# Performance work log

Hardware: AMD Instinct MI355X
Metric: run time of the kernel (lower is better)

The kernel has to match this reference:

```python
import jax, jax.numpy as jnp
import numpy as np

N = 100000      # nodes
E = 1600000     # directed edges (bidirectional pairs)
DIN = 64
DOUT = 64
T = 3
LMBDA = 0.5
EPS = 1e-9


def setup_inputs() -> dict:
    key = jax.random.key(0)
    k1, k2, k3, k4 = jax.random.split(key, 4)
    x = jax.random.normal(k1, (N, DIN), dtype=jnp.float32)
    Eh = E // 2
    s = jax.random.randint(k2, (Eh,), 0, N)
    d = jax.random.randint(k3, (Eh,), 0, N)
    # bidirectional layout required by assert_bidirectional:
    # row0 = [s, d], row1 = [d, s]
    edge_index = jnp.stack([jnp.concatenate([s, d]), jnp.concatenate([d, s])]).astype(jnp.int32)
    W = jax.random.normal(k4, (DIN, DOUT), dtype=jnp.float32) / np.sqrt(DIN)
    b = jnp.zeros((DOUT,), dtype=jnp.float32)
    lmbda = jnp.float32(LMBDA)
    return {"x": x, "edge_index": edge_index, "W": W, "b": b, "lmbda": lmbda}


def _ema(h, src, dst, lmbda):
    # h: [N, D] node features after linear; src/dst: [E] int
    Eh = src.shape[0] // 2
    deg = jax.ops.segment_sum(jnp.ones(src.shape[0], h.dtype), src, num_segments=N)  # [N]
    h_e = h[src]                       # [E, D]  (expand)
    deg_e = deg[src][:, None]          # [E, 1]
    M = h_e                            # initial edge messages M_ij = x_i
    m = jax.ops.segment_sum(M, dst, num_segments=N)  # [N, D]  (aggregate)
    coef = lmbda / (deg_e - 1.0 + EPS)

    def step(carry, _):
        M, m = carry
        m_e = m[src]                                   # [E, D]
        M_ji = jnp.roll(M, -Eh, axis=0)                # reversed-edge messages
        M_new = jnp.where(deg_e == 1.0, h_e,
                          (1.0 - lmbda) * h_e + coef * (m_e - M_ji))
        m_new = jax.ops.segment_sum(M_new, dst, num_segments=N)
        return (M_new, m_new), None

    (M, m), _ = jax.lax.scan(step, (M, m), None, length=T)
    degN = deg[:, None]
    return jnp.where(degN == 0.0, h,
                     (1.0 - lmbda) * h + lmbda / (degN + EPS) * m)


def reference(x, edge_index, W, b, lmbda):
    src, dst = edge_index[0], edge_index[1]
    x_in = x                       # dim_in == dim_out -> residual uses pre-linear x
    h = x @ W + b                  # pyg_nn.Linear
    y = jax.nn.relu(_ema(h, src, dst, lmbda))
    # dropout p=0.0 (eval) is identity
    return x_in + y
```

## Files before the change

kernel.cpp:

```cpp
#include <hip/hip_runtime.h>
#include <hip/hip_bf16.h>


static __device__ __forceinline__ float bf2f(unsigned short v) {
    union { unsigned int u; float f; } x;
    x.u = ((unsigned int)v) << 16;
    return x.f;
}

static __device__ __forceinline__ unsigned short f2bf(float f) {
    union { unsigned int u; float f; } x;
    x.f = f;
    unsigned int r = x.u + 0x7FFFu + ((x.u >> 16) & 1u);
    return (unsigned short)(r >> 16);
}

static __device__ __forceinline__ float edge_c(int dm1) {
    float fd = (float)dm1;
    float raw = 0.5f * __builtin_amdgcn_rcpf(fd);
    return (fd == 0.0f) ? 0.0f : raw;
}

__global__ void ema_gemm_kernel(const float* __restrict__ x, const float* __restrict__ W,
                                const float* __restrict__ bias, unsigned short* __restrict__ hbf) {
    int wave = (int)((blockIdx.x * 256 + threadIdx.x) >> 6);
    int lane = (int)(threadIdx.x & 63);
    int n0 = wave * 8;
    if (n0 >= 100000) return;
    float w[64];
    #pragma unroll
    for (int k = 0; k < 64; ++k) w[k] = W[k * 64 + lane];
    float bv = bias[lane];
    int nend = (n0 + 8 < 100000) ? (n0 + 8) : 100000;
    for (int n = n0; n < nend; ++n) {
        const float* xr = x + (size_t)__builtin_amdgcn_readfirstlane(n) * 64;
        float acc = bv;
        #pragma unroll
        for (int k = 0; k < 64; ++k) acc = fmaf(xr[k], w[k], acc);
        hbf[n * 64 + lane] = f2bf(acc);
    }
}

__global__ void ema_hist_kernel(const int* ei, int* hcnt) {
    __shared__ int hist[391];
    int t = (int)threadIdx.x;
    int bl = (int)blockIdx.x;
    for (int i = t; i < 391; i += 256) hist[i] = 0;
    __syncthreads();
    int e0 = bl * 4096;
    #pragma unroll
    for (int i = 0; i < 16; ++i) {
        int e = e0 + t + i * 256;
        if (e < 1600000) {
            int dst = (e < 800000) ? ei[e + 800000] : ei[e - 800000];
            atomicAdd(&hist[dst >> 8], 1);
        }
    }
    __syncthreads();
    for (int i = t; i < 391; i += 256) hcnt[i * 391 + bl] = hist[i];
}

__global__ void ema_bscan_row_kernel(int* hcnt, int* btot) {
    __shared__ int s[512];
    int bu = (int)blockIdx.x;
    int t = (int)threadIdx.x;
    int v = (t < 391) ? hcnt[bu * 391 + t] : 0;
    s[t] = v;
    __syncthreads();
    for (int off = 1; off < 512; off <<= 1) {
        int add = (t >= off) ? s[t - off] : 0;
        __syncthreads();
        s[t] += add;
        __syncthreads();
    }
    if (t < 391) hcnt[bu * 391 + t] = s[t] - v;
    if (t == 390) btot[bu] = s[t];
}

__global__ void ema_bscan_base_kernel(const int* btot, int* bbase) {
    __shared__ int s[512];
    int t = (int)threadIdx.x;
    int v = (t < 391) ? btot[t] : 0;
    s[t] = v;
    __syncthreads();
    for (int off = 1; off < 512; off <<= 1) {
        int add = (t >= off) ? s[t - off] : 0;
        __syncthreads();
        s[t] += add;
        __syncthreads();
    }
    if (t < 391) bbase[t] = s[t] - v;
    if (t == 390) bbase[391] = s[t];
}

__global__ void ema_scatter_kernel(const int* ei, const int* hcnt,
                                   const int* bbase, unsigned int* stage) {
    __shared__ int base[391];
    __shared__ int cnt[391];
    int t = (int)threadIdx.x;
    int bl = (int)blockIdx.x;
    for (int i = t; i < 391; i += 256) {
        base[i] = hcnt[i * 391 + bl] + bbase[i];
        cnt[i] = 0;
    }
    __syncthreads();
    int e0 = bl * 4096;
    #pragma unroll
    for (int i = 0; i < 16; ++i) {
        int e = e0 + t + i * 256;
        if (e < 1600000) {
            int src = ei[e];
            int dst = (e < 800000) ? ei[e + 800000] : ei[e - 800000];
            int bu = dst >> 8;
            int slot = base[bu] + atomicAdd(&cnt[bu], 1);
            stage[slot] = ((unsigned int)(dst & 255) << 24) | (unsigned int)src;
        }
    }
}

__global__ void ema_fillcsr_count_kernel(const int* __restrict__ bbase,
                                         const unsigned int* __restrict__ stage,
                                         int* __restrict__ degi,
                                         int* __restrict__ rs) {
    __shared__ int cnt[256];
    __shared__ int scn[256];
    int b = (int)blockIdx.x;
    int t = (int)threadIdx.x;
    cnt[t] = 0;
    __syncthreads();
    int seg_lo = bbase[b];
    int seg_hi = bbase[b + 1];
    for (int i = seg_lo + t; i < seg_hi; i += 256) {
        atomicAdd(&cnt[stage[i] >> 24], 1);
    }
    __syncthreads();
    int v = cnt[t];
    scn[t] = v;
    __syncthreads();
    for (int off = 1; off < 256; off <<= 1) {
        int add = (t >= off) ? scn[t - off] : 0;
        __syncthreads();
        scn[t] += add;
        __syncthreads();
    }
    int node = (b << 8) + t;
    if (node < 100000) {
        degi[node] = v;
        rs[node] = seg_lo + scn[t] - v;
    }
}

__global__ void ema_fillcsr_write_kernel(const int* __restrict__ rs,
                                         const unsigned int* __restrict__ stage,
                                         const int* __restrict__ degi,
                                         int* __restrict__ csr,
                                         float* __restrict__ cf) {
    __shared__ int rsl[256];
    __shared__ int cnt[256];
    int b = (int)blockIdx.x;
    int t = (int)threadIdx.x;
    int node_lo = b << 8;
    int node = node_lo + t;
    rsl[t] = (node < 100000) ? rs[node] : 1600000;
    cnt[t] = 0;
    __syncthreads();
    int seg_lo = rsl[0];
    int seg_hi = (node_lo + 256 < 100000) ? rs[node_lo + 256] : 1600000;
    for (int i = seg_lo + t; i < seg_hi; i += 256) {
        unsigned int v = stage[i];
        int local = (int)(v >> 24);
        int srcn = (int)(v & 0x00FFFFFFu);
        int dm1 = degi[srcn] - 1;
        if (dm1 < 0) dm1 = 0;
        if (dm1 > 32767) dm1 = 32767;
        int slot = rsl[local] + atomicAdd(&cnt[local], 1);
        csr[slot] = (dm1 << 17) | srcn;
        cf[slot] = edge_c(dm1);
    }
}

__global__ void ema_cfcopy_kernel(const float4* __restrict__ cf4,
                                  float4* __restrict__ cfD4) {
    int i = (int)(blockIdx.x * 256 + threadIdx.x);
    if (i < 400000) cfD4[i] = cf4[i];
}

__global__ void ema_passA_kernel(const int* __restrict__ degi, const int* __restrict__ rs,
                                 const int* __restrict__ csr, const float* __restrict__ cf,
                                 const unsigned short* __restrict__ hbf,
                                 unsigned short* __restrict__ m0, unsigned short* __restrict__ W1,
                                 unsigned short* __restrict__ W2, unsigned short* __restrict__ W3a,
                                 float2* __restrict__ pp) {
    int wid = (int)((blockIdx.x * 256 + threadIdx.x) >> 6);
    int c = (int)(threadIdx.x & 63);
    if (wid >= 100000) return;
    int dv = __builtin_amdgcn_readfirstlane(degi[wid]);
    int base = wid * 64 + c;
    float hv = bf2f(hbf[base]);
    if (dv == 0) {
        m0[base] = 0;
        W1[base] = 0;
        W2[base] = 0;
        W3a[base] = f2bf(hv);
        if (c == 0) pp[wid] = make_float2(0.0f, 0.0f);
        return;
    }
    int j = __builtin_amdgcn_readfirstlane(rs[wid]);
    int end = j + dv;
    float av = (dv > 1) ? 0.5f : 1.0f;
    float cv = (dv > 1) ? 0.5f / ((float)dv - 1.0f + 1e-9f) : 0.0f;
    float fv = av * hv;
    float sm = 0.0f, sS = 0.0f, sQ = 0.0f, p1 = 0.0f, p2 = 0.0f;
    for (; j + 4 <= end; j += 4) {
        unsigned int w0 = (unsigned int)csr[j];
        unsigned int w1 = (unsigned int)csr[j + 1];
        unsigned int w2 = (unsigned int)csr[j + 2];
        unsigned int w3 = (unsigned int)csr[j + 3];
        int a0 = (int)(w0 & 0x1FFFFu), d0 = (int)(w0 >> 17);
        int a1 = (int)(w1 & 0x1FFFFu), d1 = (int)(w1 >> 17);
        int a2 = (int)(w2 & 0x1FFFFu), d2 = (int)(w2 >> 17);
        int a3 = (int)(w3 & 0x1FFFFu), d3 = (int)(w3 >> 17);
        float c0 = cf[j], c1 = cf[j + 1], c2 = cf[j + 2], c3 = cf[j + 3];
        float h0 = bf2f(hbf[a0 * 64 + c]);
        float h1 = bf2f(hbf[a1 * 64 + c]);
        float h2 = bf2f(hbf[a2 * 64 + c]);
        float h3 = bf2f(hbf[a3 * 64 + c]);
        float al0 = d0 ? 0.5f : 1.0f;
        float al1 = d1 ? 0.5f : 1.0f;
        float al2 = d2 ? 0.5f : 1.0f;
        float al3 = d3 ? 0.5f : 1.0f;
        sm += (h0 + h1) + (h2 + h3);
        sS += al0 * h0 + al1 * h1 + al2 * h2 + al3 * h3;
        sQ += c0 * h0 + c1 * h1 + c2 * h2 + c3 * h3;
        p1 += (c0 + c1) + (c2 + c3);
        p2 += c0 * c0 + c1 * c1 + c2 * c2 + c3 * c3;
    }
    for (; j < end; ++j) {
        unsigned int w0 = (unsigned int)csr[j];
        int a = (int)(w0 & 0x1FFFFu), d0 = (int)(w0 >> 17);
        float ha = bf2f(hbf[a * 64 + c]);
        float ca = cf[j];
        float ala = d0 ? 0.5f : 1.0f;
        sm += ha;
        sS += ala * ha;
        sQ += ca * ha;
        p1 += ca;
        p2 += ca * ca;
    }
    float r = 0.5f / ((float)dv + 1e-9f);
    float w1o = sS - hv * p1;
    float w2o = sS - fv * p1 - cv * p1 * sm + cv * sQ;
    float w3o = 0.5f * hv + r * (sS - fv * p1 + 0.5f * cv * sQ - cv * hv * p2);
    m0[base] = f2bf(sm);
    W1[base] = f2bf(w1o);
    W2[base] = f2bf(w2o);
    W3a[base] = f2bf(w3o);
    if (c == 0) pp[wid] = make_float2(r * cv * p1, r * cv);
}

__global__ void ema_passB_kernel(const int* __restrict__ degi, const int* __restrict__ rs,
                                 const int* __restrict__ csr, const float* __restrict__ cf,
                                 const unsigned short* __restrict__ m0,
                                 unsigned short* __restrict__ W1m1, unsigned short* __restrict__ W3W4,
                                 const float2* __restrict__ pp) {
    int wid = (int)((blockIdx.x * 256 + threadIdx.x) >> 6);
    int c = (int)(threadIdx.x & 63);
    if (wid >= 100000) return;
    int dv = __builtin_amdgcn_readfirstlane(degi[wid]);
    if (dv == 0) return;
    int base = wid * 64 + c;
    int j = __builtin_amdgcn_readfirstlane(rs[wid]);
    int end = j + dv;
    float t1 = 0.0f, t2 = 0.0f;
    for (; j + 4 <= end; j += 4) {
        unsigned int w0 = (unsigned int)csr[j];
        unsigned int w1 = (unsigned int)csr[j + 1];
        unsigned int w2 = (unsigned int)csr[j + 2];
        unsigned int w3 = (unsigned int)csr[j + 3];
        int a0 = (int)(w0 & 0x1FFFFu);
        int a1 = (int)(w1 & 0x1FFFFu);
        int a2 = (int)(w2 & 0x1FFFFu);
        int a3 = (int)(w3 & 0x1FFFFu);
        float c0 = cf[j], c1 = cf[j + 1], c2 = cf[j + 2], c3 = cf[j + 3];
        float m0v = bf2f(m0[a0 * 64 + c]);
        float m1v = bf2f(m0[a1 * 64 + c]);
        float m2v = bf2f(m0[a2 * 64 + c]);
        float m3v = bf2f(m0[a3 * 64 + c]);
        t1 += c0 * m0v + c1 * m1v + c2 * m2v + c3 * m3v;
        t2 += c0 * c0 * m0v + c1 * c1 * m1v + c2 * c2 * m2v + c3 * c3 * m3v;
    }
    for (; j < end; ++j) {
        unsigned int w0 = (unsigned int)csr[j];
        int a = (int)(w0 & 0x1FFFFu);
        float ca = cf[j];
        float mv = bf2f(m0[a * 64 + c]);
        t1 += ca * mv;
        t2 += ca * ca * mv;
    }
    float2 ppv = pp[wid];
    float m1 = bf2f(W1m1[base]) + t1;
    float w4 = bf2f(W3W4[base]) - ppv.x * m1 + ppv.y * t2;
    W1m1[base] = f2bf(m1);
    W3W4[base] = f2bf(w4);
}

__global__ void ema_passC_kernel(const int* __restrict__ degi, const int* __restrict__ rs,
                                 const int* __restrict__ csr, const float* __restrict__ cf,
                                 const unsigned short* __restrict__ m1,
                                 unsigned short* __restrict__ W2m2) {
    int wid = (int)((blockIdx.x * 256 + threadIdx.x) >> 6);
    int c = (int)(threadIdx.x & 63);
    if (wid >= 100000) return;
    int dv = __builtin_amdgcn_readfirstlane(degi[wid]);
    if (dv == 0) return;
    int base = wid * 64 + c;
    int j = __builtin_amdgcn_readfirstlane(rs[wid]);
    int end = j + dv;
    float t = 0.0f;
    for (; j + 4 <= end; j += 4) {
        unsigned int w0 = (unsigned int)csr[j];
        unsigned int w1 = (unsigned int)csr[j + 1];
        unsigned int w2 = (unsigned int)csr[j + 2];
        unsigned int w3 = (unsigned int)csr[j + 3];
        int a0 = (int)(w0 & 0x1FFFFu);
        int a1 = (int)(w1 & 0x1FFFFu);
        int a2 = (int)(w2 & 0x1FFFFu);
        int a3 = (int)(w3 & 0x1FFFFu);
        float c0 = cf[j], c1 = cf[j + 1], c2 = cf[j + 2], c3 = cf[j + 3];
        float m0v = bf2f(m1[a0 * 64 + c]);
        float m1v = bf2f(m1[a1 * 64 + c]);
        float m2v = bf2f(m1[a2 * 64 + c]);
        float m3v = bf2f(m1[a3 * 64 + c]);
        t += c0 * m0v + c1 * m1v + c2 * m2v + c3 * m3v;
    }
    for (; j < end; ++j) {
        unsigned int w0 = (unsigned int)csr[j];
        int a = (int)(w0 & 0x1FFFFu);
        t += cf[j] * bf2f(m1[a * 64 + c]);
    }
    float m2v = bf2f(W2m2[base]) + t;
    W2m2[base] = f2bf(m2v);
}

__global__ void GraphEMALayer_18133351924067_kernel(
    const int* __restrict__ degi, const int* __restrict__ rs,
    const int* __restrict__ csr, const float* __restrict__ cfD,
    const unsigned short* __restrict__ m2, const unsigned short* __restrict__ W4,
    const float* __restrict__ x, float* __restrict__ out) {
    int wid = (int)((blockIdx.x * 256 + threadIdx.x) >> 6);
    int c = (int)(threadIdx.x & 63);
    if (wid >= 100000) return;
    int dv = __builtin_amdgcn_readfirstlane(degi[wid]);
    int base = wid * 64 + c;
    float xv = x[base];
    float y = bf2f(W4[base]);
    if (dv > 0) {
        int j = __builtin_amdgcn_readfirstlane(rs[wid]);
        int end = j + dv;
        float t = 0.0f;
        for (; j + 4 <= end; j += 4) {
            unsigned int w0 = (unsigned int)csr[j];
            unsigned int w1 = (unsigned int)csr[j + 1];
            unsigned int w2 = (unsigned int)csr[j + 2];
            unsigned int w3 = (unsigned int)csr[j + 3];
            int a0 = (int)(w0 & 0x1FFFFu);
            int a1 = (int)(w1 & 0x1FFFFu);
            int a2 = (int)(w2 & 0x1FFFFu);
            int a3 = (int)(w3 & 0x1FFFFu);
            float c0 = cfD[j], c1 = cfD[j + 1], c2 = cfD[j + 2], c3 = cfD[j + 3];
            float m0v = bf2f(m2[a0 * 64 + c]);
            float m1v = bf2f(m2[a1 * 64 + c]);
            float m2v = bf2f(m2[a2 * 64 + c]);
            float m3v = bf2f(m2[a3 * 64 + c]);
            t += c0 * m0v + c1 * m1v + c2 * m2v + c3 * m3v;
        }
        for (; j < end; ++j) {
            unsigned int w0 = (unsigned int)csr[j];
            int a = (int)(w0 & 0x1FFFFu);
            t += cfD[j] * bf2f(m2[a * 64 + c]);
        }
        float r = 0.5f / ((float)dv + 1e-9f);
        y += r * t;
    }
    if (y < 0.0f) y = 0.0f;
    out[base] = xv + y;
}

extern "C" void kernel_launch(void* const* d_in, const int* in_sizes, int n_in,
                              void* d_out, int out_size, void* d_ws, size_t ws_size,
                              hipStream_t stream) {
    (void)in_sizes; (void)n_in; (void)out_size; (void)ws_size;

    const float* x    = (const float*)d_in[0];
    const int*   ei   = (const int*)d_in[1];
    const float* W    = (const float*)d_in[2];
    const float* bias = (const float*)d_in[3];
    float* out = (float*)d_out;
    unsigned short* m0 = (unsigned short*)d_out;
    float* cf = (float*)((char*)d_out + 12800000);

    char* ws = (char*)d_ws;
    unsigned short* hbf  = (unsigned short*)(ws);
    unsigned short* W1m1 = (unsigned short*)(ws + 12800000);
    unsigned short* W2m2 = (unsigned short*)(ws + 25600000);
    unsigned short* W3W4 = (unsigned short*)(ws + 38400000);
    int* degi = (int*)(ws + 51200000);
    int* rs   = (int*)(ws + 51600000);
    float2* pp   = (float2*)(ws + 52800000);
    int* csr  = (int*)(ws + 53600000);
    int* bbase = (int*)(ws + 60000000);
    int* btot  = (int*)(ws + 60002048);

    unsigned int* stage = (unsigned int*)(ws + 12800000);
    int* hcnt = (int*)(ws + 25600000);
    float* cfD = (float*)(ws);

    int eb = (100000 * 64 + 255) / 256;
    int nb = (100000 + 255) / 256;
    int pb = (1600000 + 4095) / 4096;
    int gb = (100000 + 31) / 32;
    int cb = (400000 + 255) / 256;

    ema_gemm_kernel<<<gb, 256, 0, stream>>>(x, W, bias, hbf);

    ema_hist_kernel<<<pb, 256, 0, stream>>>(ei, hcnt);
    ema_bscan_row_kernel<<<391, 512, 0, stream>>>(hcnt, btot);
    ema_bscan_base_kernel<<<1, 512, 0, stream>>>(btot, bbase);
    ema_scatter_kernel<<<pb, 256, 0, stream>>>(ei, hcnt, bbase, stage);
    ema_fillcsr_count_kernel<<<nb, 256, 0, stream>>>(bbase, stage, degi, rs);
    ema_fillcsr_write_kernel<<<nb, 256, 0, stream>>>(rs, stage, degi, csr, cf);

    ema_passA_kernel<<<eb, 256, 0, stream>>>(degi, rs, csr, cf, hbf,
                                             m0, W1m1, W2m2, W3W4, pp);
    ema_cfcopy_kernel<<<cb, 256, 0, stream>>>((const float4*)cf, (float4*)cfD);
    ema_passB_kernel<<<eb, 256, 0, stream>>>(degi, rs, csr, cf, m0,
                                             W1m1, W3W4, pp);
    ema_passC_kernel<<<eb, 256, 0, stream>>>(degi, rs, csr, cf, W1m1, W2m2);
    GraphEMALayer_18133351924067_kernel<<<eb, 256, 0, stream>>>(
        degi, rs, csr, cfD, W2m2, W3W4, x, out);
}
```

Baseline: 387.3 us.

## Merge CSR count/write, precompute edge coefficients and squared coefficients, unroll gathers by eight

The two CSR fill kernels are merged into one that keeps the row starts in shared memory, and the packed degree bits are dropped from csr. A new kernel computes per-edge coefficients and their squares, and another computes the per-node p1/p2 sums with wave reductions, which moves that work out of passA. The gather loops in all passes are unrolled to 8 edges to keep more loads in flight. This adds two kernel launches and an extra cf2 array read in passB, in exchange for fewer serial dependencies and less per-edge arithmetic.

```diff
diff --git a/kernel.cpp b/kernel.cpp
--- a/kernel.cpp
+++ b/kernel.cpp
@@ -118,12 +118,14 @@
     }
 }
 
-__global__ void ema_fillcsr_count_kernel(const int* __restrict__ bbase,
-                                         const unsigned int* __restrict__ stage,
-                                         int* __restrict__ degi,
-                                         int* __restrict__ rs) {
+__global__ void ema_fillcsr_kernel(const int* __restrict__ bbase,
+                                   const unsigned int* __restrict__ stage,
+                                   int* __restrict__ degi,
+                                   int* __restrict__ rs,
+                                   int* __restrict__ csr) {
     __shared__ int cnt[256];
     __shared__ int scn[256];
+    __shared__ int rsl[256];
     int b = (int)blockIdx.x;
     int t = (int)threadIdx.x;
     cnt[t] = 0;
@@ -143,40 +145,58 @@
         scn[t] += add;
         __syncthreads();
     }
+    int start = seg_lo + scn[t] - v;
+    rsl[t] = start;
     int node = (b << 8) + t;
     if (node < 100000) {
         degi[node] = v;
-        rs[node] = seg_lo + scn[t] - v;
-    }
-}
-
-__global__ void ema_fillcsr_write_kernel(const int* __restrict__ rs,
-                                         const unsigned int* __restrict__ stage,
-                                         const int* __restrict__ degi,
-                                         int* __restrict__ csr,
-                                         float* __restrict__ cf) {
-    __shared__ int rsl[256];
-    __shared__ int cnt[256];
-    int b = (int)blockIdx.x;
-    int t = (int)threadIdx.x;
-    int node_lo = b << 8;
-    int node = node_lo + t;
-    rsl[t] = (node < 100000) ? rs[node] : 1600000;
+        rs[node] = start;
+    }
     cnt[t] = 0;
     __syncthreads();
-    int seg_lo = rsl[0];
-    int seg_hi = (node_lo + 256 < 100000) ? rs[node_lo + 256] : 1600000;
     for (int i = seg_lo + t; i < seg_hi; i += 256) {
-        unsigned int v = stage[i];
-        int local = (int)(v >> 24);
-        int srcn = (int)(v & 0x00FFFFFFu);
-        int dm1 = degi[srcn] - 1;
-        if (dm1 < 0) dm1 = 0;
-        if (dm1 > 32767) dm1 = 32767;
+        unsigned int s = stage[i];
+        int local = (int)(s >> 24);
+        int srcn = (int)(s & 0x00FFFFFFu);
         int slot = rsl[local] + atomicAdd(&cnt[local], 1);
-        csr[slot] = (dm1 << 17) | srcn;
-        cf[slot] = edge_c(dm1);
-    }
+        csr[slot] = srcn;
+    }
+}
+
+__global__ void ema_cfgen_kernel(const int* __restrict__ csr,
+                                 const int* __restrict__ degi,
+                                 float* __restrict__ cf,
+                                 float* __restrict__ cf2) {
+    int i = (int)(blockIdx.x * 256 + threadIdx.x);
+    if (i >= 1600000) return;
+    int dm1 = degi[csr[i]] - 1;
+    float v = edge_c(dm1);
+    cf[i] = v;
+    cf2[i] = v * v;
+}
+
+__global__ void ema_p12_kernel(const int* __restrict__ degi, const int* __restrict__ rs,
+                               const float* __restrict__ cf, float2* __restrict__ P12) {
+    int wid = (int)((blockIdx.x * 256 + threadIdx.x) >> 6);
+    int lane = (int)(threadIdx.x & 63);
+    if (wid >= 100000) return;
+    int dv = __builtin_amdgcn_readfirstlane(degi[wid]);
+    if (dv == 0) {
+        if (lane == 0) P12[wid] = make_float2(0.0f, 0.0f);
+        return;
+    }
+    int j0 = __builtin_amdgcn_readfirstlane(rs[wid]);
+    float p1 = 0.0f, p2 = 0.0f;
+    for (int l = lane; l < dv; l += 64) {
+        float cv = cf[j0 + l];
+        p1 += cv;
+        p2 += cv * cv;
+    }
+    for (int off = 32; off > 0; off >>= 1) {
+        p1 += __shfl_xor(p1, off);
+        p2 += __shfl_xor(p2, off);
+    }
+    if (lane == 0) P12[wid] = make_float2(p1, p2);
 }
 
 __global__ void ema_cfcopy_kernel(const float4* __restrict__ cf4,
@@ -187,6 +207,7 @@
 
 __global__ void ema_passA_kernel(const int* __restrict__ degi, const int* __restrict__ rs,
                                  const int* __restrict__ csr, const float* __restrict__ cf,
+                                 const float2* __restrict__ P12,
                                  const unsigned short* __restrict__ hbf,
                                  unsigned short* __restrict__ m0, unsigned short* __restrict__ W1,
                                  unsigned short* __restrict__ W2, unsigned short* __restrict__ W3a,
@@ -210,42 +231,59 @@
     float av = (dv > 1) ? 0.5f : 1.0f;
     float cv = (dv > 1) ? 0.5f / ((float)dv - 1.0f + 1e-9f) : 0.0f;
     float fv = av * hv;
-    float sm = 0.0f, sS = 0.0f, sQ = 0.0f, p1 = 0.0f, p2 = 0.0f;
+    float2 p12 = P12[wid];
+    float p1 = p12.x, p2 = p12.y;
+    float sm = 0.0f, sS = 0.0f, sQ = 0.0f;
+    for (; j + 8 <= end; j += 8) {
+        int a0 = csr[j],     a1 = csr[j + 1], a2 = csr[j + 2], a3 = csr[j + 3];
+        int a4 = csr[j + 4], a5 = csr[j + 5], a6 = csr[j + 6], a7 = csr[j + 7];
+        float c0 = cf[j],     c1 = cf[j + 1], c2 = cf[j + 2], c3 = cf[j + 3];
+        float c4 = cf[j + 4], c5 = cf[j + 5], c6 = cf[j + 6], c7 = cf[j + 7];
+        float h0 = bf2f(hbf[a0 * 64 + c]);
+        float h1 = bf2f(hbf[a1 * 64 + c]);
+        float h2 = bf2f(hbf[a2 * 64 + c]);
+        float h3 = bf2f(hbf[a3 * 64 + c]);
+        float h4 = bf2f(hbf[a4 * 64 + c]);
+        float h5 = bf2f(hbf[a5 * 64 + c]);
+        float h6 = bf2f(hbf[a6 * 64 + c]);
+        float h7 = bf2f(hbf[a7 * 64 + c]);
+        float al0 = (c0 == 0.0f) ? 1.0f : 0.5f;
+        float al1 = (c1 == 0.0f) ? 1.0f : 0.5f;
+        float al2 = (c2 == 0.0f) ? 1.0f : 0.5f;
+        float al3 = (c3 == 0.0f) ? 1.0f : 0.5f;
+        float al4 = (c4 == 0.0f) ? 1.0f : 0.5f;
+        float al5 = (c5 == 0.0f) ? 1.0f : 0.5f;
+        float al6 = (c6 == 0.0f) ? 1.0f : 0.5f;
+        float al7 = (c7 == 0.0f) ? 1.0f : 0.5f;
+        sm += ((h0 + h1) + (h2 + h3)) + ((h4 + h5) + (h6 + h7));
+        sS += (al0 * h0 + al1 * h1 + al2 * h2 + al3 * h3)
+            + (al4 * h4 + al5 * h5 + al6 * h6 + al7 * h7);
+        sQ += (c0 * h0 + c1 * h1 + c2 * h2 + c3 * h3)
+            + (c4 * h4 + c5 * h5 + c6 * h6 + c7 * h7);
+    }
     for (; j + 4 <= end; j += 4) {
-        unsigned int w0 = (unsigned int)csr[j];
-        unsigned int w1 = (unsigned int)csr[j + 1];
-        unsigned int w2 = (unsigned int)csr[j + 2];
-        unsigned int w3 = (unsigned int)csr[j + 3];
-        int a0 = (int)(w0 & 0x1FFFFu), d0 = (int)(w0 >> 17);
-        int a1 = (int)(w1 & 0x1FFFFu), d1 = (int)(w1 >> 17);
-        int a2 = (int)(w2 & 0x1FFFFu), d2 = (int)(w2 >> 17);
-        int a3 = (int)(w3 & 0x1FFFFu), d3 = (int)(w3 >> 17);
+        int a0 = csr[j], a1 = csr[j + 1], a2 = csr[j + 2], a3 = csr[j + 3];
         float c0 = cf[j], c1 = cf[j + 1], c2 = cf[j + 2], c3 = cf[j + 3];
         float h0 = bf2f(hbf[a0 * 64 + c]);
         float h1 = bf2f(hbf[a1 * 64 + c]);
         float h2 = bf2f(hbf[a2 * 64 + c]);
         float h3 = bf2f(hbf[a3 * 64 + c]);
-        float al0 = d0 ? 0.5f : 1.0f;
-        float al1 = d1 ? 0.5f : 1.0f;
-        float al2 = d2 ? 0.5f : 1.0f;
-        float al3 = d3 ? 0.5f : 1.0f;
+        float al0 = (c0 == 0.0f) ? 1.0f : 0.5f;
+        float al1 = (c1 == 0.0f) ? 1.0f : 0.5f;
+        float al2 = (c2 == 0.0f) ? 1.0f : 0.5f;
+        float al3 = (c3 == 0.0f) ? 1.0f : 0.5f;
         sm += (h0 + h1) + (h2 + h3);
         sS += al0 * h0 + al1 * h1 + al2 * h2 + al3 * h3;
         sQ += c0 * h0 + c1 * h1 + c2 * h2 + c3 * h3;
-        p1 += (c0 + c1) + (c2 + c3);
-        p2 += c0 * c0 + c1 * c1 + c2 * c2 + c3 * c3;
     }
     for (; j < end; ++j) {
-        unsigned int w0 = (unsigned int)csr[j];
-        int a = (int)(w0 & 0x1FFFFu), d0 = (int)(w0 >> 17);
+        int a = csr[j];
+        float ca = cf[j];
         float ha = bf2f(hbf[a * 64 + c]);
-        float ca = cf[j];
-        float ala = d0 ? 0.5f : 1.0f;
+        float ala = (ca == 0.0f) ? 1.0f : 0.5f;
         sm += ha;
         sS += ala * ha;
         sQ += ca * ha;
-        p1 += ca;
-        p2 += ca * ca;
     }
     float r = 0.5f / ((float)dv + 1e-9f);
     float w1o = sS - hv * p1;
@@ -260,6 +298,7 @@
 
 __global__ void ema_passB_kernel(const int* __restrict__ degi, const int* __restrict__ rs,
                                  const int* __restrict__ csr, const float* __restrict__ cf,
+                                 const float* __restrict__ cf2,
                                  const unsigned short* __restrict__ m0,
                                  unsigned short* __restrict__ W1m1, unsigned short* __restrict__ W3W4,
                                  const float2* __restrict__ pp) {
@@ -272,30 +311,42 @@
     int j = __builtin_amdgcn_readfirstlane(rs[wid]);
     int end = j + dv;
     float t1 = 0.0f, t2 = 0.0f;
+    for (; j + 8 <= end; j += 8) {
+        int a0 = csr[j],     a1 = csr[j + 1], a2 = csr[j + 2], a3 = csr[j + 3];
+        int a4 = csr[j + 4], a5 = csr[j + 5], a6 = csr[j + 6], a7 = csr[j + 7];
+        float c0 = cf[j],     c1 = cf[j + 1], c2 = cf[j + 2], c3 = cf[j + 3];
+        float c4 = cf[j + 4], c5 = cf[j + 5], c6 = cf[j + 6], c7 = cf[j + 7];
+        float q0 = cf2[j],     q1 = cf2[j + 1], q2 = cf2[j + 2], q3 = cf2[j + 3];
+        float q4 = cf2[j + 4], q5 = cf2[j + 5], q6 = cf2[j + 6], q7 = cf2[j + 7];
+        float v0 = bf2f(m0[a0 * 64 + c]);
+        float v1 = bf2f(m0[a1 * 64 + c]);
+        float v2 = bf2f(m0[a2 * 64 + c]);
+        float v3 = bf2f(m0[a3 * 64 + c]);
+        float v4 = bf2f(m0[a4 * 64 + c]);
+        float v5 = bf2f(m0[a5 * 64 + c]);
+        float v6 = bf2f(m0[a6 * 64 + c]);
+        float v7 = bf2f(m0[a7 * 64 + c]);
+        t1 += (c0 * v0 + c1 * v1 + c2 * v2 + c3 * v3)
+            + (c4 * v4 + c5 * v5 + c6 * v6 + c7 * v7);
+        t2 += (q0 * v0 + q1 * v1 + q2 * v2 + q3 * v3)
+            + (q4 * v4 + q5 * v5 + q6 * v6 + q7 * v7);
+    }
     for (; j + 4 <= end; j += 4) {
-        unsigned int w0 = (unsigned int)csr[j];
-        unsigned int w1 = (unsigned int)csr[j + 1];
-        unsigned int w2 = (unsigned int)csr[j + 2];
-        unsigned int w3 = (unsigned int)csr[j + 3];
-        int a0 = (int)(w0 & 0x1FFFFu);
-        int a1 = (int)(w1 & 0x1FFFFu);
-        int a2 = (int)(w2 & 0x1FFFFu);
-        int a3 = (int)(w3 & 0x1FFFFu);
+        int a0 = csr[j], a1 = csr[j + 1], a2 = csr[j + 2], a3 = csr[j + 3];
         float c0 = cf[j], c1 = cf[j + 1], c2 = cf[j + 2], c3 = cf[j + 3];
-        float m0v = bf2f(m0[a0 * 64 + c]);
-        float m1v = bf2f(m0[a1 * 64 + c]);
-        float m2v = bf2f(m0[a2 * 64 + c]);
-        float m3v = bf2f(m0[a3 * 64 + c]);
-        t1 += c0 * m0v + c1 * m1v + c2 * m2v + c3 * m3v;
-        t2 += c0 * c0 * m0v + c1 * c1 * m1v + c2 * c2 * m2v + c3 * c3 * m3v;
+        float q0 = cf2[j], q1 = cf2[j + 1], q2 = cf2[j + 2], q3 = cf2[j + 3];
+        float v0 = bf2f(m0[a0 * 64 + c]);
+        float v1 = bf2f(m0[a1 * 64 + c]);
+        float v2 = bf2f(m0[a2 * 64 + c]);
+        float v3 = bf2f(m0[a3 * 64 + c]);
+        t1 += c0 * v0 + c1 * v1 + c2 * v2 + c3 * v3;
+        t2 += q0 * v0 + q1 * v1 + q2 * v2 + q3 * v3;
     }
     for (; j < end; ++j) {
-        unsigned int w0 = (unsigned int)csr[j];
-        int a = (int)(w0 & 0x1FFFFu);
-        float ca = cf[j];
+        int a = csr[j];
         float mv = bf2f(m0[a * 64 + c]);
-        t1 += ca * mv;
-        t2 += ca * ca * mv;
+        t1 += cf[j] * mv;
+        t2 += cf2[j] * mv;
     }
     float2 ppv = pp[wid];
     float m1 = bf2f(W1m1[base]) + t1;
@@ -317,25 +368,33 @@
     int j = __builtin_amdgcn_readfirstlane(rs[wid]);
     int end = j + dv;
     float t = 0.0f;
+    for (; j + 8 <= end; j += 8) {
+        int a0 = csr[j],     a1 = csr[j + 1], a2 = csr[j + 2], a3 = csr[j + 3];
+        int a4 = csr[j + 4], a5 = csr[j + 5], a6 = csr[j + 6], a7 = csr[j + 7];
+        float c0 = cf[j],     c1 = cf[j + 1], c2 = cf[j + 2], c3 = cf[j + 3];
+        float c4 = cf[j + 4], c5 = cf[j + 5], c6 = cf[j + 6], c7 = cf[j + 7];
+        float v0 = bf2f(m1[a0 * 64 + c]);
+        float v1 = bf2f(m1[a1 * 64 + c]);
+        float v2 = bf2f(m1[a2 * 64 + c]);
+        float v3 = bf2f(m1[a3 * 64 + c]);
+        float v4 = bf2f(m1[a4 * 64 + c]);
+        float v5 = bf2f(m1[a5 * 64 + c]);
+        float v6 = bf2f(m1[a6 * 64 + c]);
+        float v7 = bf2f(m1[a7 * 64 + c]);
+        t += (c0 * v0 + c1 * v1 + c2 * v2 + c3 * v3)
+           + (c4 * v4 + c5 * v5 + c6 * v6 + c7 * v7);
+    }
     for (; j + 4 <= end; j += 4) {
-        unsigned int w0 = (unsigned int)csr[j];
-        unsigned int w1 = (unsigned int)csr[j + 1];
-        unsigned int w2 = (unsigned int)csr[j + 2];
-        unsigned int w3 = (unsigned int)csr[j + 3];
-        int a0 = (int)(w0 & 0x1FFFFu);
-        int a1 = (int)(w1 & 0x1FFFFu);
-        int a2 = (int)(w2 & 0x1FFFFu);
-        int a3 = (int)(w3 & 0x1FFFFu);
+        int a0 = csr[j], a1 = csr[j + 1], a2 = csr[j + 2], a3 = csr[j + 3];
         float c0 = cf[j], c1 = cf[j + 1], c2 = cf[j + 2], c3 = cf[j + 3];
-        float m0v = bf2f(m1[a0 * 64 + c]);
-        float m1v = bf2f(m1[a1 * 64 + c]);
-        float m2v = bf2f(m1[a2 * 64 + c]);
-        float m3v = bf2f(m1[a3 * 64 + c]);
-        t += c0 * m0v + c1 * m1v + c2 * m2v + c3 * m3v;
+        float v0 = bf2f(m1[a0 * 64 + c]);
+        float v1 = bf2f(m1[a1 * 64 + c]);
+        float v2 = bf2f(m1[a2 * 64 + c]);
+        float v3 = bf2f(m1[a3 * 64 + c]);
+        t += c0 * v0 + c1 * v1 + c2 * v2 + c3 * v3;
     }
     for (; j < end; ++j) {
-        unsigned int w0 = (unsigned int)csr[j];
-        int a = (int)(w0 & 0x1FFFFu);
+        int a = csr[j];
         t += cf[j] * bf2f(m1[a * 64 + c]);
     }
     float m2v = bf2f(W2m2[base]) + t;
@@ -358,25 +417,33 @@
         int j = __builtin_amdgcn_readfirstlane(rs[wid]);
         int end = j + dv;
         float t = 0.0f;
+        for (; j + 8 <= end; j += 8) {
+            int a0 = csr[j],     a1 = csr[j + 1], a2 = csr[j + 2], a3 = csr[j + 3];
+            int a4 = csr[j + 4], a5 = csr[j + 5], a6 = csr[j + 6], a7 = csr[j + 7];
+            float c0 = cfD[j],     c1 = cfD[j + 1], c2 = cfD[j + 2], c3 = cfD[j + 3];
+            float c4 = cfD[j + 4], c5 = cfD[j + 5], c6 = cfD[j + 6], c7 = cfD[j + 7];
+            float v0 = bf2f(m2[a0 * 64 + c]);
+            float v1 = bf2f(m2[a1 * 64 + c]);
+            float v2 = bf2f(m2[a2 * 64 + c]);
+            float v3 = bf2f(m2[a3 * 64 + c]);
+            float v4 = bf2f(m2[a4 * 64 + c]);
+            float v5 = bf2f(m2[a5 * 64 + c]);
+            float v6 = bf2f(m2[a6 * 64 + c]);
+            float v7 = bf2f(m2[a7 * 64 + c]);
+            t += (c0 * v0 + c1 * v1 + c2 * v2 + c3 * v3)
+               + (c4 * v4 + c5 * v5 + c6 * v6 + c7 * v7);
+        }
         for (; j + 4 <= end; j += 4) {
-            unsigned int w0 = (unsigned int)csr[j];
-            unsigned int w1 = (unsigned int)csr[j + 1];
-            unsigned int w2 = (unsigned int)csr[j + 2];
-            unsigned int w3 = (unsigned int)csr[j + 3];
-            int a0 = (int)(w0 & 0x1FFFFu);
-            int a1 = (int)(w1 & 0x1FFFFu);
-            int a2 = (int)(w2 & 0x1FFFFu);
-            int a3 = (int)(w3 & 0x1FFFFu);
+            int a0 = csr[j], a1 = csr[j + 1], a2 = csr[j + 2], a3 = csr[j + 3];
             float c0 = cfD[j], c1 = cfD[j + 1], c2 = cfD[j + 2], c3 = cfD[j + 3];
-            float m0v = bf2f(m2[a0 * 64 + c]);
-            float m1v = bf2f(m2[a1 * 64 + c]);
-            float m2v = bf2f(m2[a2 * 64 + c]);
-            float m3v = bf2f(m2[a3 * 64 + c]);
-            t += c0 * m0v + c1 * m1v + c2 * m2v + c3 * m3v;
+            float v0 = bf2f(m2[a0 * 64 + c]);
+            float v1 = bf2f(m2[a1 * 64 + c]);
+            float v2 = bf2f(m2[a2 * 64 + c]);
+            float v3 = bf2f(m2[a3 * 64 + c]);
+            t += c0 * v0 + c1 * v1 + c2 * v2 + c3 * v3;
         }
         for (; j < end; ++j) {
-            unsigned int w0 = (unsigned int)csr[j];
-            int a = (int)(w0 & 0x1FFFFu);
+            int a = csr[j];
             t += cfD[j] * bf2f(m2[a * 64 + c]);
         }
         float r = 0.5f / ((float)dv + 1e-9f);
@@ -397,7 +464,8 @@
     const float* bias = (const float*)d_in[3];
     float* out = (float*)d_out;
     unsigned short* m0 = (unsigned short*)d_out;
-    float* cf = (float*)((char*)d_out + 12800000);
+    float* cf  = (float*)((char*)d_out + 12800000);
+    float* cf2 = (float*)((char*)d_out + 19200000);
 
     char* ws = (char*)d_ws;
     unsigned short* hbf  = (unsigned short*)(ws);
@@ -406,7 +474,8 @@
     unsigned short* W3W4 = (unsigned short*)(ws + 38400000);
     int* degi = (int*)(ws + 51200000);
     int* rs   = (int*)(ws + 51600000);
-    float2* pp   = (float2*)(ws + 52800000);
+    float2* P12 = (float2*)(ws + 52000000);
+    float2* pp  = (float2*)(ws + 52800000);
     int* csr  = (int*)(ws + 53600000);
     int* bbase = (int*)(ws + 60000000);
     int* btot  = (int*)(ws + 60002048);
@@ -419,6 +488,7 @@
     int nb = (100000 + 255) / 256;
     int pb = (1600000 + 4095) / 4096;
     int gb = (100000 + 31) / 32;
+    int db = (1600000 + 255) / 256;
     int cb = (400000 + 255) / 256;
 
     ema_gemm_kernel<<<gb, 256, 0, stream>>>(x, W, bias, hbf);
@@ -427,13 +497,14 @@
     ema_bscan_row_kernel<<<391, 512, 0, stream>>>(hcnt, btot);
     ema_bscan_base_kernel<<<1, 512, 0, stream>>>(btot, bbase);
     ema_scatter_kernel<<<pb, 256, 0, stream>>>(ei, hcnt, bbase, stage);
-    ema_fillcsr_count_kernel<<<nb, 256, 0, stream>>>(bbase, stage, degi, rs);
-    ema_fillcsr_write_kernel<<<nb, 256, 0, stream>>>(rs, stage, degi, csr, cf);
-
-    ema_passA_kernel<<<eb, 256, 0, stream>>>(degi, rs, csr, cf, hbf,
+    ema_fillcsr_kernel<<<nb, 256, 0, stream>>>(bbase, stage, degi, rs, csr);
+    ema_cfgen_kernel<<<db, 256, 0, stream>>>(csr, degi, cf, cf2);
+    ema_p12_kernel<<<eb, 256, 0, stream>>>(degi, rs, cf, P12);
+
+    ema_passA_kernel<<<eb, 256, 0, stream>>>(degi, rs, csr, cf, P12, hbf,
                                              m0, W1m1, W2m2, W3W4, pp);
     ema_cfcopy_kernel<<<cb, 256, 0, stream>>>((const float4*)cf, (float4*)cfD);
-    ema_passB_kernel<<<eb, 256, 0, stream>>>(degi, rs, csr, cf, m0,
+    ema_passB_kernel<<<eb, 256, 0, stream>>>(degi, rs, csr, cf, cf2, m0,
                                              W1m1, W3W4, pp);
     ema_passC_kernel<<<eb, 256, 0, stream>>>(degi, rs, csr, cf, W1m1, W2m2);
     GraphEMALayer_18133351924067_kernel<<<eb, 256, 0, stream>>>(
```

Result: faster. 375.4 us (-3.1%).
